# Performance work log

Measured on AMD Instinct MI355X. Metric: run time of the kernel, lower is better.

The kernel has to match this reference:

```python
import jax, jax.numpy as jnp
import numpy as np

ST_HIDDEN = 128
ST_HEADS = 4
ST_LAYERS = 3
RES_SCALE = 1.0
DK = ST_HIDDEN // ST_HEADS


def build_3d_adj(spatial_ei, spatial_ea, n_nodes, window):
    # replicate spatial edges per time slice with node offset t*n_nodes
    offs = (jnp.arange(window) * n_nodes)[None, :, None]  # [1,W,1]
    all_sp_idx = (spatial_ei[:, None, :] + offs).reshape(2, -1)  # [2, W*E]
    all_sp_attr = jnp.tile(spatial_ea, (window, 1))  # [W*E, De]
    # temporal edges t -> t+1 for every node
    src = jnp.arange((window - 1) * n_nodes)
    temp_idx = jnp.stack([src, src + n_nodes], axis=0)  # [2, (W-1)*N]
    temp_attr = jnp.broadcast_to(spatial_ea.mean(axis=0, keepdims=True),
                                 (temp_idx.shape[1], spatial_ea.shape[1]))
    ei = jnp.concatenate([all_sp_idx, temp_idx], axis=1)
    ea = jnp.concatenate([all_sp_attr, temp_attr], axis=0)
    return ei, ea


def seg_softmax(logits, dst, num_nodes):
    # logits [E,H], segment softmax over dst (pyg_softmax)
    m = jax.ops.segment_max(logits, dst, num_segments=num_nodes)  # [N,H]
    ex = jnp.exp(logits - m[dst])
    s = jax.ops.segment_sum(ex, dst, num_segments=num_nodes)
    return ex / (s[dst] + 1e-16)


def layernorm(x, g, b, eps=1e-5):
    mu = x.mean(-1, keepdims=True)
    var = ((x - mu) ** 2).mean(-1, keepdims=True)
    return (x - mu) * jax.lax.rsqrt(var + eps) * g + b


def block(x, ei, ea, qw, qb, kw, kb, vw, vb, fw, fb, ow, ob, ln_g, ln_b):
    B, Nt, _ = x.shape
    H, dk = ST_HEADS, DK
    Q = (x @ qw + qb).reshape(B, Nt, H, dk)
    K = (x @ kw + kb).reshape(B, Nt, H, dk)
    V = (x @ vw + vb).reshape(B, Nt, H, dk)
    src, dst = ei[0], ei[1]
    q_e = Q[:, dst]  # [B,E,H,dk]
    k_e = K[:, src]
    v_e = V[:, src]
    film = ea @ fw + fb  # [E, 2*hidden]
    gamma, beta = jnp.split(film, 2, axis=-1)
    gamma = gamma.reshape(1, -1, H, dk)
    beta = beta.reshape(1, -1, H, dk)
    k_e = k_e * (1.0 + gamma) + beta
    logits = (q_e * k_e).sum(-1) / np.sqrt(dk).astype(np.float32)  # [B,E,H]
    att = jax.vmap(lambda l: seg_softmax(l, dst, Nt))(logits)
    msg = att[..., None] * v_e  # [B,E,H,dk]
    out = jnp.zeros((B, Nt, H, dk), x.dtype).at[:, dst].add(msg)
    y = out.reshape(B, Nt, H * dk) @ ow + ob
    return layernorm(x + y, ln_g, ln_b)


def setup_inputs() -> dict:
    key = jax.random.key(0)
    ks = jax.random.split(key, 12)
    B, W, N, Fin, E, De = 2, 16, 1000, 16, 16000, 8
    H, L = ST_HIDDEN, ST_LAYERS
    g = lambda k, s: jax.random.normal(k, s, jnp.float32) * 0.05
    return {
        "xw": jax.random.normal(ks[0], (B, W, N, Fin), jnp.float32),
        "spatial_ei": jax.random.randint(ks[1], (2, E), 0, N),
        "spatial_ea": jax.random.normal(ks[2], (E, De), jnp.float32),
        "in_w": g(ks[3], (Fin, H)), "in_b": jnp.zeros((H,), jnp.float32),
        "qw": g(ks[4], (L, H, H)), "qb": jnp.zeros((L, H), jnp.float32),
        "kw": g(ks[5], (L, H, H)), "kb": jnp.zeros((L, H), jnp.float32),
        "vw": g(ks[6], (L, H, H)), "vb": jnp.zeros((L, H), jnp.float32),
        "fw": g(ks[7], (L, De, 2 * H)), "fb": jnp.zeros((L, 2 * H), jnp.float32),
        "ow": g(ks[8], (L, H, H)), "ob": jnp.zeros((L, H), jnp.float32),
        "ln_g": jnp.ones((L, H), jnp.float32), "ln_b": jnp.zeros((L, H), jnp.float32),
        "head_w": g(ks[9], (H, 1)), "head_b": jnp.zeros((1,), jnp.float32),
    }


def reference(xw, spatial_ei, spatial_ea, in_w, in_b, qw, qb, kw, kb, vw, vb,
              fw, fb, ow, ob, ln_g, ln_b, head_w, head_b):
    B, W, N, Fin = xw.shape
    ei, ea = build_3d_adj(spatial_ei, spatial_ea, N, W)
    x = xw.reshape(B, W * N, Fin) @ in_w + in_b
    for l in range(ST_LAYERS):
        bx = block(x, ei, ea, qw[l], qb[l], kw[l], kb[l], vw[l], vb[l],
                   fw[l], fb[l], ow[l], ob[l], ln_g[l], ln_b[l])
        x = x + RES_SCALE * (bx - x)
    last = x.reshape(B, W, N, -1)[:, -1]  # [B,N,H]
    return jax.nn.softplus(last @ head_w + head_b).squeeze(-1)  # [B,N]
```

## Files before the change

### kernel.cpp

```cpp
#include <hip/hip_runtime.h>
#include <math.h>

constexpr int B    = 2;
constexpr int W    = 16;
constexpr int N    = 1000;
constexpr int FIN  = 16;
constexpr int E    = 16000;
constexpr int DE   = 8;
constexpr int H    = 128;
constexpr int L    = 3;
constexpr int WL   = 4;
constexpr int W0G  = 12;
constexpr int RPB  = WL * N;
constexpr int ROWS = B * RPB;
constexpr int NMAT = 12;

__device__ __forceinline__ float blockSum128(float v) {
  #pragma unroll
  for (int off = 32; off >= 1; off >>= 1) v += __shfl_xor(v, off);
  __shared__ float s2[2];
  int w = threadIdx.x >> 6;
  __syncthreads();
  if ((threadIdx.x & 63) == 0) s2[w] = v;
  __syncthreads();
  return s2[0] + s2[1];
}

__device__ __forceinline__ float dpp_add_xor1(float x) {
  int y = __builtin_amdgcn_update_dpp(0, __float_as_int(x), 0xB1, 0xF, 0xF, true);
  return x + __int_as_float(y);
}
__device__ __forceinline__ float dpp_add_xor2(float x) {
  int y = __builtin_amdgcn_update_dpp(0, __float_as_int(x), 0x4E, 0xF, 0xF, true);
  return x + __int_as_float(y);
}
__device__ __forceinline__ float headSum32(float p) {
  p = dpp_add_xor1(p);
  p = dpp_add_xor2(p);
  p += __shfl_xor(p, 4);
  p += __shfl_xor(p, 8);
  p += __shfl_xor(p, 16);
  return p;
}
__device__ __forceinline__ float dot4(float4 a, float4 b) {
  return a.x * b.x + a.y * b.y + a.z * b.z + a.w * b.w;
}

__global__ void k_count_scan(const int* __restrict__ ei, int* __restrict__ offs,
                             int* __restrict__ cursor, float* __restrict__ meanea) {
  __shared__ int cnt[N];
  __shared__ int scn[1024];
  int t = threadIdx.x;
  if (t < 8) meanea[t] = 0.f;
  if (t < N) cnt[t] = 0;
  __syncthreads();
  int vals[16];
  int nv = 0;
  for (int e = t; e < E; e += 1024) vals[nv++] = ei[E + e];
  for (int i = 0; i < nv; i++) atomicAdd(&cnt[vals[i]], 1);
  __syncthreads();
  int v = (t < N) ? cnt[t] : 0;
  scn[t] = v;
  __syncthreads();
  for (int st = 1; st < 1024; st <<= 1) {
    int add = (t >= st) ? scn[t - st] : 0;
    __syncthreads();
    scn[t] += add;
    __syncthreads();
  }
  if (t < N) {
    offs[t + 1] = scn[t];
    if (t == 0) offs[0] = 0;
    cursor[t] = scn[t] - v;
  }
}

__global__ void k_prep2(const int* __restrict__ ei, const float* __restrict__ ea,
                        int* __restrict__ cursor, int2* __restrict__ csr,
                        float* __restrict__ meanea,
                        const float* __restrict__ qw, const float* __restrict__ kw,
                        const float* __restrict__ vw, const float* __restrict__ ow,
                        float4* __restrict__ wTp4,
                        const float* __restrict__ xw, const float* __restrict__ in_w,
                        const float* __restrict__ in_b, float* __restrict__ x) {
  int bid = blockIdx.x;
  int t = threadIdx.x;
  if (bid < 64) {
    int e = bid * 256 + t;
    if (e < E) {
      int src = ei[e];
      int dst = ei[E + e];
      int pos = atomicAdd(&cursor[dst], 1);
      csr[pos] = make_int2(src, e);
    }
  } else if (bid < 128) {
    __shared__ float sbuf[256];
    int d = t & 7, g = t >> 3;
    float s = 0.f;
    for (int e = (bid - 64) * 32 + g; e < E; e += 64 * 32) s += ea[e * DE + d];
    sbuf[t] = s;
    __syncthreads();
    for (int st = 16; st >= 1; st >>= 1) {
      if (g < st) sbuf[g * 8 + d] += sbuf[(g + st) * 8 + d];
      __syncthreads();
    }
    if (g == 0) atomicAdd(&meanea[d], sbuf[d]);
  } else if (bid < 128 + NMAT * 16) {
    int bid2 = bid - 128;
    int mat = bid2 / 16;
    int pair = bid2 % 16;
    int kk4 = pair * 2 + (t >> 7);
    int c = t & 127;
    int l = mat >> 2, mm = mat & 3;
    const float* src = ((mm == 0) ? qw : (mm == 1) ? kw : (mm == 2) ? vw : ow) + (long)l * H * H;
    int k0 = kk4 * 4;
    float4 v4;
    v4.x = src[(k0 + 0) * H + c];
    v4.y = src[(k0 + 1) * H + c];
    v4.z = src[(k0 + 2) * H + c];
    v4.w = src[(k0 + 3) * H + c];
    wTp4[((long)mat * 32 + kk4) * H + c] = v4;
  } else {
    int bi = bid - (128 + NMAT * 16);
    int b = bi / 63, tt = bi % 63;
    int lr0 = tt * 64;
    __shared__ float xwS[64][FIN];
    __shared__ float inS[FIN][H];
    for (int i = t; i < 64 * FIN; i += 256) {
      int r = i >> 4, k = i & 15;
      int lr = lr0 + r;
      float val = 0.f;
      if (lr < RPB) {
        int wl = lr / N, n = lr % N;
        val = xw[(((long)b * W + (W0G + wl)) * N + n) * FIN + k];
      }
      xwS[r][k] = val;
    }
    for (int i = t; i < FIN * H; i += 256) inS[i >> 7][i & 127] = in_w[i];
    __syncthreads();
    #pragma unroll
    for (int qi = 0; qi < 8; qi++) {
      int idx = t + qi * 256;
      int r = idx >> 5, cq = idx & 31;
      int lr = lr0 + r;
      if (lr < RPB) {
        float4 acc = *(const float4*)(in_b + cq * 4);
        #pragma unroll
        for (int k = 0; k < FIN; k++) {
          float xv = xwS[r][k];
          float4 w4 = *(const float4*)(&inS[k][cq * 4]);
          acc.x += xv * w4.x; acc.y += xv * w4.y; acc.z += xv * w4.z; acc.w += xv * w4.w;
        }
        *(float4*)(x + ((long)b * RPB + lr) * H + cq * 4) = acc;
      }
    }
  }
}

__global__ void k_film(const float* __restrict__ ea, const float* __restrict__ fw,
                       const float* __restrict__ fb, const float* __restrict__ meanea,
                       unsigned int* __restrict__ filmh) {
  int e0 = blockIdx.x * 4;
  int t = threadIdx.x;
  float rgw[DE], rbw[DE];
  #pragma unroll
  for (int d = 0; d < DE; d++) {
    rgw[d] = fw[d * 2 * H + t];
    rbw[d] = fw[d * 2 * H + H + t];
  }
  float fbg = fb[t], fbb = fb[H + t];
  for (int e = e0; e < e0 + 4 && e <= E; e++) {
    float a[DE];
    if (e < E) {
      float4 a0 = *(const float4*)(ea + (long)e * DE);
      float4 a1 = *(const float4*)(ea + (long)e * DE + 4);
      a[0] = a0.x; a[1] = a0.y; a[2] = a0.z; a[3] = a0.w;
      a[4] = a1.x; a[5] = a1.y; a[6] = a1.z; a[7] = a1.w;
    } else {
      #pragma unroll
      for (int d = 0; d < DE; d++) a[d] = meanea[d] * (1.0f / E);
    }
    float g = fbg, be = fbb;
    #pragma unroll
    for (int d = 0; d < DE; d++) {
      g  += a[d] * rgw[d];
      be += a[d] * rbw[d];
    }
    unsigned int gb = __float_as_uint(g);
    gb = (gb + 0x7fffu + ((gb >> 16) & 1u)) >> 16;
    unsigned int bb_ = __float_as_uint(be);
    bb_ = (bb_ + 0x7fffu + ((bb_ >> 16) & 1u)) & 0xffff0000u;
    filmh[(long)e * H + t] = gb | bb_;
  }
}

__global__ void k_gemm(const float* __restrict__ X, const float4* __restrict__ wTp4,
                       int matBase,
                       const float* __restrict__ bq, const float* __restrict__ bk,
                       const float* __restrict__ bv,
                       float* __restrict__ Cq, float* __restrict__ Ck, float* __restrict__ Cv,
                       int base, int rows_pb, int tiles) {
  int m = blockIdx.y;
  const float* bm = (m == 0) ? bq : (m == 1) ? bk : bv;
  float* Cm       = (m == 0) ? Cq : (m == 1) ? Ck : Cv;
  const float4* wp = wTp4 + (long)(matBase + m) * 32 * H;
  int bb = blockIdx.x / tiles;
  int tt = blockIdx.x % tiles;
  int lr0 = tt * 32;
  long grow0 = (long)bb * RPB + base + lr0;
  int t = threadIdx.x;
  __shared__ float xs[32][H];
  #pragma unroll
  for (int qi = 0; qi < 4; qi++) {
    int idx = t + qi * 256;
    int r = idx >> 5, c4 = idx & 31;
    float4 v4 = make_float4(0.f, 0.f, 0.f, 0.f);
    if (lr0 + r < rows_pb) v4 = *(const float4*)(X + (grow0 + r) * H + c4 * 4);
    *(float4*)&xs[r][c4 * 4] = v4;
  }
  __syncthreads();
  int cg = t & 31, rg = t >> 5;
  float4 bias4 = *(const float4*)(bm + cg * 4);
  float4 acc0 = bias4, acc1 = bias4, acc2 = bias4, acc3 = bias4;
  #pragma unroll 4
  for (int kk4 = 0; kk4 < 32; kk4++) {
    const float4* wr = wp + kk4 * H + cg * 4;
    float4 w0 = wr[0], w1 = wr[1], w2 = wr[2], w3 = wr[3];
    float4 x0 = *(const float4*)&xs[rg * 4 + 0][kk4 * 4];
    float4 x1 = *(const float4*)&xs[rg * 4 + 1][kk4 * 4];
    float4 x2 = *(const float4*)&xs[rg * 4 + 2][kk4 * 4];
    float4 x3 = *(const float4*)&xs[rg * 4 + 3][kk4 * 4];
    acc0.x += dot4(x0, w0); acc0.y += dot4(x0, w1); acc0.z += dot4(x0, w2); acc0.w += dot4(x0, w3);
    acc1.x += dot4(x1, w0); acc1.y += dot4(x1, w1); acc1.z += dot4(x1, w2); acc1.w += dot4(x1, w3);
    acc2.x += dot4(x2, w0); acc2.y += dot4(x2, w1); acc2.z += dot4(x2, w2); acc2.w += dot4(x2, w3);
    acc3.x += dot4(x3, w0); acc3.y += dot4(x3, w1); acc3.z += dot4(x3, w2); acc3.w += dot4(x3, w3);
  }
  int lrr = lr0 + rg * 4;
  if (lrr + 0 < rows_pb) *(float4*)(Cm + (grow0 + rg * 4 + 0) * H + cg * 4) = acc0;
  if (lrr + 1 < rows_pb) *(float4*)(Cm + (grow0 + rg * 4 + 1) * H + cg * 4) = acc1;
  if (lrr + 2 < rows_pb) *(float4*)(Cm + (grow0 + rg * 4 + 2) * H + cg * 4) = acc2;
  if (lrr + 3 < rows_pb) *(float4*)(Cm + (grow0 + rg * 4 + 3) * H + cg * 4) = acc3;
}

__global__ void k_attn_oln(const float* __restrict__ Qb, const float* __restrict__ Kb,
                           const float* __restrict__ Vb,
                           const unsigned int* __restrict__ filmh,
                           const int* __restrict__ offs, const int2* __restrict__ csr,
                           const float* __restrict__ x, const float4* __restrict__ owp,
                           const float* __restrict__ ob, const float* __restrict__ lng,
                           const float* __restrict__ lnb, float* __restrict__ xo,
                           int out_lo,
                           const float* __restrict__ hw, const float* __restrict__ hb,
                           float* __restrict__ out, int do_head) {
  int tid = threadIdx.x;
  int nwin = WL - out_lo;
  int idx = blockIdx.x;
  int b = idx / (nwin * N);
  int rem = idx % (nwin * N);
  int wl = out_lo + rem / N;
  int n = rem % N;
  long drow = ((long)b * WL + wl) * N + n;
  float q = Qb[drow * H + tid];
  long sbase = ((long)b * WL + wl) * N;
  long trow  = ((long)b * WL + wl - 1) * N + n;
  const float scale = 0.17677669529663687f;
  int i0 = offs[n], i1 = offs[n + 1];

  unsigned int fh = filmh[(long)E * H + tid];
  float g  = __uint_as_float(fh << 16);
  float be = __uint_as_float(fh & 0xffff0000u);
  float kv = Kb[trow * H + tid];
  float vv = Vb[trow * H + tid];
  float p  = q * (kv * (1.f + g) + be);
  float pe = __expf(headSum32(p) * scale);
  float ssum = pe, acc = pe * vv;

  for (int i4 = i0; i4 < i1; i4 += 4) {
    #pragma unroll
    for (int j = 0; j < 4; j++) {
      int i = i4 + j;
      int ic = (i < i1) ? i : (i1 - 1);
      int2 se = csr[ic];
      long srow = sbase + se.x;
      unsigned int f2 = filmh[(long)se.y * H + tid];
      float g2 = __uint_as_float(f2 << 16);
      float b2 = __uint_as_float(f2 & 0xffff0000u);
      float kv2 = Kb[srow * H + tid];
      float vv2 = Vb[srow * H + tid];
      float p2  = q * (kv2 * (1.f + g2) + b2);
      float pe2 = __expf(headSum32(p2) * scale);
      pe2 = (i < i1) ? pe2 : 0.f;
      ssum += pe2;
      acc  += pe2 * vv2;
    }
  }
  float ab = acc / (ssum + 1e-16f);

  __shared__ float sab[H];
  sab[tid] = ab;
  __syncthreads();
  float y = ob[tid];
  #pragma unroll 8
  for (int kk4 = 0; kk4 < 32; kk4++) {
    float4 w4 = owp[kk4 * H + tid];
    float4 a4 = *(const float4*)&sab[kk4 * 4];
    y += dot4(a4, w4);
  }

  float v = x[drow * H + tid] + y;
  float mu = blockSum128(v) * (1.f / H);
  float dv = v - mu;
  float var = blockSum128(dv * dv) * (1.f / H);
  float o = dv * rsqrtf(var + 1e-5f) * lng[tid] + lnb[tid];

  if (!do_head) {
    xo[drow * H + tid] = o;
  } else {
    float hv = o * hw[tid];
    float tot = blockSum128(hv);
    if (tid == 0) {
      float z = tot + hb[0];
      out[b * N + n] = fmaxf(z, 0.f) + log1pf(expf(-fabsf(z)));
    }
  }
}

extern "C" void kernel_launch(void* const* d_in, const int* in_sizes, int n_in,
                              void* d_out, int out_size, void* d_ws, size_t ws_size,
                              hipStream_t stream) {
  const float* xw   = (const float*)d_in[0];
  const int*   ei   = (const int*)d_in[1];
  const float* ea   = (const float*)d_in[2];
  const float* in_w = (const float*)d_in[3];
  const float* in_b = (const float*)d_in[4];
  const float* qw   = (const float*)d_in[5];
  const float* qb   = (const float*)d_in[6];
  const float* kw   = (const float*)d_in[7];
  const float* kb   = (const float*)d_in[8];
  const float* vw   = (const float*)d_in[9];
  const float* vb   = (const float*)d_in[10];
  const float* fw   = (const float*)d_in[11];
  const float* fb   = (const float*)d_in[12];
  const float* ow   = (const float*)d_in[13];
  const float* ob   = (const float*)d_in[14];
  const float* ln_g = (const float*)d_in[15];
  const float* ln_b = (const float*)d_in[16];
  const float* hw   = (const float*)d_in[17];
  const float* hb   = (const float*)d_in[18];
  float* out = (float*)d_out;

  float* ws   = (float*)d_ws;
  float* x    = ws;
  float* x2   = x  + (long)ROWS * H;
  float* Qb   = x2 + (long)ROWS * H;
  float* Kb   = Qb + (long)ROWS * H;
  float* Vb   = Kb + (long)ROWS * H;
  float* wTp  = Vb + (long)ROWS * H;
  unsigned int* filmh = (unsigned int*)(wTp + (long)NMAT * H * H);
  float* meanea = (float*)(filmh + (long)(E + 1) * H);
  int* offs    = (int*)(meanea + 8);
  int* cursor  = offs + N + 1;
  int2* csr    = (int2*)(cursor + N);
  float4* wTp4 = (float4*)wTp;

  k_count_scan<<<1, 1024, 0, stream>>>(ei, offs, cursor, meanea);
  k_prep2<<<128 + NMAT * 16 + 126, 256, 0, stream>>>(
      ei, ea, cursor, csr, meanea, qw, kw, vw, ow, wTp4, xw, in_w, in_b, x);

  float* xa = x;
  float* xb = x2;
  for (int l = 0; l < L; l++) {
    int in_lo = l, out_lo = l + 1;
    k_film<<<(E + 1 + 3) / 4, 128, 0, stream>>>(
        ea, fw + (long)l * DE * 2 * H, fb + (long)l * 2 * H, meanea, filmh);
    int rows_pb = (WL - in_lo) * N;
    int tiles = (rows_pb + 31) / 32;
    k_gemm<<<dim3(B * tiles, 3), 256, 0, stream>>>(
        xa, wTp4, l * 4, qb + (long)l * H, kb + (long)l * H, vb + (long)l * H,
        Qb, Kb, Vb, in_lo * N, rows_pb, tiles);
    int nout = B * (WL - out_lo) * N;
    int last = (l == L - 1) ? 1 : 0;
    k_attn_oln<<<nout, H, 0, stream>>>(
        Qb, Kb, Vb, filmh, offs, csr,
        xa, wTp4 + ((long)l * 4 + 3) * 32 * H, ob + (long)l * H,
        ln_g + (long)l * H, ln_b + (long)l * H, xb, out_lo,
        hw, hb, out, last);
    float* tmp = xa; xa = xb; xb = tmp;
  }
}
```

Before: 268.5 us.

## Precompute FiLM for all layers in prep, pack four nodes per attention block

The per-layer FiLM kernel is removed. FiLM coefficients for all three layers are now computed once inside the prep kernel and stored in a three-layer buffer, and the edge-attribute mean moves into a second block of the count/scan kernel so prep can read it without atomics. The attention/out-proj/LayerNorm kernel now processes four destination nodes per 512-thread block, using a grouped block reduction in place of one node per 128-thread block. This cuts kernel launches and small-block scheduling overhead, at the cost of more workspace and a larger prep kernel.

```diff
diff --git a/kernel.cpp b/kernel.cpp
--- a/kernel.cpp
+++ b/kernel.cpp
@@ -14,17 +14,9 @@
 constexpr int RPB  = WL * N;
 constexpr int ROWS = B * RPB;
 constexpr int NMAT = 12;
-
-__device__ __forceinline__ float blockSum128(float v) {
-  #pragma unroll
-  for (int off = 32; off >= 1; off >>= 1) v += __shfl_xor(v, off);
-  __shared__ float s2[2];
-  int w = threadIdx.x >> 6;
-  __syncthreads();
-  if ((threadIdx.x & 63) == 0) s2[w] = v;
-  __syncthreads();
-  return s2[0] + s2[1];
-}
+constexpr int FB   = (E + 1 + 7) / 8;
+constexpr int NPB  = 4;
+constexpr int NG   = N / NPB;
 
 __device__ __forceinline__ float dpp_add_xor1(float x) {
   int y = __builtin_amdgcn_update_dpp(0, __float_as_int(x), 0xB1, 0xF, 0xF, true);
@@ -45,13 +37,36 @@
 __device__ __forceinline__ float dot4(float4 a, float4 b) {
   return a.x * b.x + a.y * b.y + a.z * b.z + a.w * b.w;
 }
+__device__ __forceinline__ float grpSum128(float v, int tid, int g) {
+  #pragma unroll
+  for (int off = 32; off >= 1; off >>= 1) v += __shfl_xor(v, off);
+  __shared__ float sred[8];
+  __syncthreads();
+  if ((tid & 63) == 0) sred[tid >> 6] = v;
+  __syncthreads();
+  return sred[g * 2] + sred[g * 2 + 1];
+}
 
 __global__ void k_count_scan(const int* __restrict__ ei, int* __restrict__ offs,
-                             int* __restrict__ cursor, float* __restrict__ meanea) {
+                             int* __restrict__ cursor,
+                             const float* __restrict__ ea, float* __restrict__ meanea) {
+  int t = threadIdx.x;
+  if (blockIdx.x == 1) {
+    __shared__ float sbuf[1024];
+    int d = t & 7, g = t >> 3;
+    float s = 0.f;
+    for (int e = g; e < E; e += 128) s += ea[(long)e * DE + d];
+    sbuf[t] = s;
+    __syncthreads();
+    for (int st = 64; st >= 1; st >>= 1) {
+      if (g < st) sbuf[g * 8 + d] += sbuf[(g + st) * 8 + d];
+      __syncthreads();
+    }
+    if (g == 0) meanea[d] = sbuf[d];
+    return;
+  }
   __shared__ int cnt[N];
   __shared__ int scn[1024];
-  int t = threadIdx.x;
-  if (t < 8) meanea[t] = 0.f;
   if (t < N) cnt[t] = 0;
   __syncthreads();
   int vals[16];
@@ -77,12 +92,14 @@
 
 __global__ void k_prep2(const int* __restrict__ ei, const float* __restrict__ ea,
                         int* __restrict__ cursor, int2* __restrict__ csr,
-                        float* __restrict__ meanea,
+                        const float* __restrict__ meanea,
                         const float* __restrict__ qw, const float* __restrict__ kw,
                         const float* __restrict__ vw, const float* __restrict__ ow,
                         float4* __restrict__ wTp4,
                         const float* __restrict__ xw, const float* __restrict__ in_w,
-                        const float* __restrict__ in_b, float* __restrict__ x) {
+                        const float* __restrict__ in_b, float* __restrict__ x,
+                        const float* __restrict__ fw, const float* __restrict__ fb,
+                        unsigned int* __restrict__ filmh) {
   int bid = blockIdx.x;
   int t = threadIdx.x;
   if (bid < 64) {
@@ -93,20 +110,8 @@
       int pos = atomicAdd(&cursor[dst], 1);
       csr[pos] = make_int2(src, e);
     }
-  } else if (bid < 128) {
-    __shared__ float sbuf[256];
-    int d = t & 7, g = t >> 3;
-    float s = 0.f;
-    for (int e = (bid - 64) * 32 + g; e < E; e += 64 * 32) s += ea[e * DE + d];
-    sbuf[t] = s;
-    __syncthreads();
-    for (int st = 16; st >= 1; st >>= 1) {
-      if (g < st) sbuf[g * 8 + d] += sbuf[(g + st) * 8 + d];
-      __syncthreads();
-    }
-    if (g == 0) atomicAdd(&meanea[d], sbuf[d]);
-  } else if (bid < 128 + NMAT * 16) {
-    int bid2 = bid - 128;
+  } else if (bid < 64 + NMAT * 16) {
+    int bid2 = bid - 64;
     int mat = bid2 / 16;
     int pair = bid2 % 16;
     int kk4 = pair * 2 + (t >> 7);
@@ -120,8 +125,8 @@
     v4.z = src[(k0 + 2) * H + c];
     v4.w = src[(k0 + 3) * H + c];
     wTp4[((long)mat * 32 + kk4) * H + c] = v4;
-  } else {
-    int bi = bid - (128 + NMAT * 16);
+  } else if (bid < 64 + NMAT * 16 + 126) {
+    int bi = bid - (64 + NMAT * 16);
     int b = bi / 63, tt = bi % 63;
     int lr0 = tt * 64;
     __shared__ float xwS[64][FIN];
@@ -154,43 +159,46 @@
         *(float4*)(x + ((long)b * RPB + lr) * H + cq * 4) = acc;
       }
     }
-  }
-}
-
-__global__ void k_film(const float* __restrict__ ea, const float* __restrict__ fw,
-                       const float* __restrict__ fb, const float* __restrict__ meanea,
-                       unsigned int* __restrict__ filmh) {
-  int e0 = blockIdx.x * 4;
-  int t = threadIdx.x;
-  float rgw[DE], rbw[DE];
-  #pragma unroll
-  for (int d = 0; d < DE; d++) {
-    rgw[d] = fw[d * 2 * H + t];
-    rbw[d] = fw[d * 2 * H + H + t];
-  }
-  float fbg = fb[t], fbb = fb[H + t];
-  for (int e = e0; e < e0 + 4 && e <= E; e++) {
-    float a[DE];
-    if (e < E) {
-      float4 a0 = *(const float4*)(ea + (long)e * DE);
-      float4 a1 = *(const float4*)(ea + (long)e * DE + 4);
-      a[0] = a0.x; a[1] = a0.y; a[2] = a0.z; a[3] = a0.w;
-      a[4] = a1.x; a[5] = a1.y; a[6] = a1.z; a[7] = a1.w;
-    } else {
-      #pragma unroll
-      for (int d = 0; d < DE; d++) a[d] = meanea[d] * (1.0f / E);
-    }
-    float g = fbg, be = fbb;
+  } else {
+    int fi = bid - (64 + NMAT * 16 + 126);
+    int l = fi / FB;
+    int blk = fi % FB;
+    int ch = t & 127;
+    int eg = t >> 7;
+    const float* fwl = fw + (long)l * DE * 2 * H;
+    const float* fbl = fb + (long)l * 2 * H;
+    unsigned int* fh = filmh + (long)l * (E + 1) * H;
+    float rgw[DE], rbw[DE];
     #pragma unroll
     for (int d = 0; d < DE; d++) {
-      g  += a[d] * rgw[d];
-      be += a[d] * rbw[d];
-    }
-    unsigned int gb = __float_as_uint(g);
-    gb = (gb + 0x7fffu + ((gb >> 16) & 1u)) >> 16;
-    unsigned int bb_ = __float_as_uint(be);
-    bb_ = (bb_ + 0x7fffu + ((bb_ >> 16) & 1u)) & 0xffff0000u;
-    filmh[(long)e * H + t] = gb | bb_;
+      rgw[d] = fwl[d * 2 * H + ch];
+      rbw[d] = fwl[d * 2 * H + H + ch];
+    }
+    float fbg = fbl[ch], fbb = fbl[H + ch];
+    int e0 = blk * 8 + eg * 4;
+    for (int e = e0; e < e0 + 4 && e <= E; e++) {
+      float a[DE];
+      if (e < E) {
+        float4 a0 = *(const float4*)(ea + (long)e * DE);
+        float4 a1 = *(const float4*)(ea + (long)e * DE + 4);
+        a[0] = a0.x; a[1] = a0.y; a[2] = a0.z; a[3] = a0.w;
+        a[4] = a1.x; a[5] = a1.y; a[6] = a1.z; a[7] = a1.w;
+      } else {
+        #pragma unroll
+        for (int d = 0; d < DE; d++) a[d] = meanea[d] * (1.0f / E);
+      }
+      float g = fbg, be = fbb;
+      #pragma unroll
+      for (int d = 0; d < DE; d++) {
+        g  += a[d] * rgw[d];
+        be += a[d] * rbw[d];
+      }
+      unsigned int gb = __float_as_uint(g);
+      gb = (gb + 0x7fffu + ((gb >> 16) & 1u)) >> 16;
+      unsigned int bb_ = __float_as_uint(be);
+      bb_ = (bb_ + 0x7fffu + ((bb_ >> 16) & 1u)) & 0xffff0000u;
+      fh[(long)e * H + ch] = gb | bb_;
+    }
   }
 }
 
@@ -253,25 +261,27 @@
                            const float* __restrict__ hw, const float* __restrict__ hb,
                            float* __restrict__ out, int do_head) {
   int tid = threadIdx.x;
+  int g   = tid >> 7;
+  int ch  = tid & 127;
   int nwin = WL - out_lo;
   int idx = blockIdx.x;
-  int b = idx / (nwin * N);
-  int rem = idx % (nwin * N);
-  int wl = out_lo + rem / N;
-  int n = rem % N;
+  int b = idx / (nwin * NG);
+  int rem = idx % (nwin * NG);
+  int wl = out_lo + rem / NG;
+  int n = (rem % NG) * NPB + g;
   long drow = ((long)b * WL + wl) * N + n;
-  float q = Qb[drow * H + tid];
+  float q = Qb[drow * H + ch];
   long sbase = ((long)b * WL + wl) * N;
   long trow  = ((long)b * WL + wl - 1) * N + n;
   const float scale = 0.17677669529663687f;
   int i0 = offs[n], i1 = offs[n + 1];
 
-  unsigned int fh = filmh[(long)E * H + tid];
-  float g  = __uint_as_float(fh << 16);
+  unsigned int fh = filmh[(long)E * H + ch];
+  float gg = __uint_as_float(fh << 16);
   float be = __uint_as_float(fh & 0xffff0000u);
-  float kv = Kb[trow * H + tid];
-  float vv = Vb[trow * H + tid];
-  float p  = q * (kv * (1.f + g) + be);
+  float kv = Kb[trow * H + ch];
+  float vv = Vb[trow * H + ch];
+  float p  = q * (kv * (1.f + gg) + be);
   float pe = __expf(headSum32(p) * scale);
   float ssum = pe, acc = pe * vv;
 
@@ -282,11 +292,11 @@
       int ic = (i < i1) ? i : (i1 - 1);
       int2 se = csr[ic];
       long srow = sbase + se.x;
-      unsigned int f2 = filmh[(long)se.y * H + tid];
+      unsigned int f2 = filmh[(long)se.y * H + ch];
       float g2 = __uint_as_float(f2 << 16);
       float b2 = __uint_as_float(f2 & 0xffff0000u);
-      float kv2 = Kb[srow * H + tid];
-      float vv2 = Vb[srow * H + tid];
+      float kv2 = Kb[srow * H + ch];
+      float vv2 = Vb[srow * H + ch];
       float p2  = q * (kv2 * (1.f + g2) + b2);
       float pe2 = __expf(headSum32(p2) * scale);
       pe2 = (i < i1) ? pe2 : 0.f;
@@ -296,29 +306,29 @@
   }
   float ab = acc / (ssum + 1e-16f);
 
-  __shared__ float sab[H];
-  sab[tid] = ab;
-  __syncthreads();
-  float y = ob[tid];
+  __shared__ float sab[NPB][H];
+  sab[g][ch] = ab;
+  __syncthreads();
+  float y = ob[ch];
   #pragma unroll 8
   for (int kk4 = 0; kk4 < 32; kk4++) {
-    float4 w4 = owp[kk4 * H + tid];
-    float4 a4 = *(const float4*)&sab[kk4 * 4];
+    float4 w4 = owp[kk4 * H + ch];
+    float4 a4 = *(const float4*)&sab[g][kk4 * 4];
     y += dot4(a4, w4);
   }
 
-  float v = x[drow * H + tid] + y;
-  float mu = blockSum128(v) * (1.f / H);
+  float v = x[drow * H + ch] + y;
+  float mu = grpSum128(v, tid, g) * (1.f / H);
   float dv = v - mu;
-  float var = blockSum128(dv * dv) * (1.f / H);
-  float o = dv * rsqrtf(var + 1e-5f) * lng[tid] + lnb[tid];
+  float var = grpSum128(dv * dv, tid, g) * (1.f / H);
+  float o = dv * rsqrtf(var + 1e-5f) * lng[ch] + lnb[ch];
 
   if (!do_head) {
-    xo[drow * H + tid] = o;
+    xo[drow * H + ch] = o;
   } else {
-    float hv = o * hw[tid];
-    float tot = blockSum128(hv);
-    if (tid == 0) {
+    float hv = o * hw[ch];
+    float tot = grpSum128(hv, tid, g);
+    if (ch == 0) {
       float z = tot + hb[0];
       out[b * N + n] = fmaxf(z, 0.f) + log1pf(expf(-fabsf(z)));
     }
@@ -357,31 +367,30 @@
   float* Vb   = Kb + (long)ROWS * H;
   float* wTp  = Vb + (long)ROWS * H;
   unsigned int* filmh = (unsigned int*)(wTp + (long)NMAT * H * H);
-  float* meanea = (float*)(filmh + (long)(E + 1) * H);
+  int2* csr    = (int2*)(filmh + 3L * (E + 1) * H);
+  float* meanea = (float*)(csr + E);
   int* offs    = (int*)(meanea + 8);
   int* cursor  = offs + N + 1;
-  int2* csr    = (int2*)(cursor + N);
   float4* wTp4 = (float4*)wTp;
 
-  k_count_scan<<<1, 1024, 0, stream>>>(ei, offs, cursor, meanea);
-  k_prep2<<<128 + NMAT * 16 + 126, 256, 0, stream>>>(
-      ei, ea, cursor, csr, meanea, qw, kw, vw, ow, wTp4, xw, in_w, in_b, x);
+  k_count_scan<<<2, 1024, 0, stream>>>(ei, offs, cursor, ea, meanea);
+  k_prep2<<<64 + NMAT * 16 + 126 + 3 * FB, 256, 0, stream>>>(
+      ei, ea, cursor, csr, meanea, qw, kw, vw, ow, wTp4, xw, in_w, in_b, x,
+      fw, fb, filmh);
 
   float* xa = x;
   float* xb = x2;
   for (int l = 0; l < L; l++) {
     int in_lo = l, out_lo = l + 1;
-    k_film<<<(E + 1 + 3) / 4, 128, 0, stream>>>(
-        ea, fw + (long)l * DE * 2 * H, fb + (long)l * 2 * H, meanea, filmh);
     int rows_pb = (WL - in_lo) * N;
     int tiles = (rows_pb + 31) / 32;
     k_gemm<<<dim3(B * tiles, 3), 256, 0, stream>>>(
         xa, wTp4, l * 4, qb + (long)l * H, kb + (long)l * H, vb + (long)l * H,
         Qb, Kb, Vb, in_lo * N, rows_pb, tiles);
-    int nout = B * (WL - out_lo) * N;
+    int nout = B * (WL - out_lo) * NG;
     int last = (l == L - 1) ? 1 : 0;
-    k_attn_oln<<<nout, H, 0, stream>>>(
-        Qb, Kb, Vb, filmh, offs, csr,
+    k_attn_oln<<<nout, NPB * H, 0, stream>>>(
+        Qb, Kb, Vb, filmh + (long)l * (E + 1) * H, offs, csr,
         xa, wTp4 + ((long)l * 4 + 3) * 32 * H, ob + (long)l * H,
         ln_g + (long)l * H, ln_b + (long)l * H, xb, out_lo,
         hw, hb, out, last);
```

Measured after the change: 290.6 us. +8.2%, slower.

## Precompute FiLM for all layers in prep kernel and parallelize edge histogram

Applied to the files above, without the earlier changes.

The three per-layer k_film launches are removed; FiLM gamma/beta for all three layers are now computed up front as extra blocks of k_prep2 and stored in a tripled filmh buffer indexed per layer. The single-block count+scan kernel is split into a multi-block global-atomic histogram (which also does the ea mean), preceded by a memset and followed by a single-block scan. This cuts launches inside the layer loop and spreads the histogram across many blocks. The cost is one more memset and scan launch up front and a larger workspace.

```diff
diff --git a/kernel.cpp b/kernel.cpp
--- a/kernel.cpp
+++ b/kernel.cpp
@@ -14,6 +14,7 @@
 constexpr int RPB  = WL * N;
 constexpr int ROWS = B * RPB;
 constexpr int NMAT = 12;
+constexpr int FB   = (E + 1 + 7) / 8;
 
 __device__ __forceinline__ float blockSum128(float v) {
   #pragma unroll
@@ -46,19 +47,32 @@
   return a.x * b.x + a.y * b.y + a.z * b.z + a.w * b.w;
 }
 
-__global__ void k_count_scan(const int* __restrict__ ei, int* __restrict__ offs,
-                             int* __restrict__ cursor, float* __restrict__ meanea) {
-  __shared__ int cnt[N];
+__global__ void k_hist(const int* __restrict__ ei, int* __restrict__ cnt,
+                       const float* __restrict__ ea, float* __restrict__ meanea) {
+  int bid = blockIdx.x;
+  int t = threadIdx.x;
+  if (bid < 64) {
+    int e = bid * 256 + t;
+    if (e < E) atomicAdd(&cnt[ei[E + e]], 1);
+  } else {
+    __shared__ float sbuf[256];
+    int d = t & 7, g = t >> 3;
+    float s = 0.f;
+    for (int e = (bid - 64) * 32 + g; e < E; e += 64 * 32) s += ea[(long)e * DE + d];
+    sbuf[t] = s;
+    __syncthreads();
+    for (int st = 16; st >= 1; st >>= 1) {
+      if (g < st) sbuf[g * 8 + d] += sbuf[(g + st) * 8 + d];
+      __syncthreads();
+    }
+    if (g == 0) atomicAdd(&meanea[d], sbuf[d]);
+  }
+}
+
+__global__ void k_scan(const int* __restrict__ cnt, int* __restrict__ offs,
+                       int* __restrict__ cursor) {
   __shared__ int scn[1024];
   int t = threadIdx.x;
-  if (t < 8) meanea[t] = 0.f;
-  if (t < N) cnt[t] = 0;
-  __syncthreads();
-  int vals[16];
-  int nv = 0;
-  for (int e = t; e < E; e += 1024) vals[nv++] = ei[E + e];
-  for (int i = 0; i < nv; i++) atomicAdd(&cnt[vals[i]], 1);
-  __syncthreads();
   int v = (t < N) ? cnt[t] : 0;
   scn[t] = v;
   __syncthreads();
@@ -77,12 +91,14 @@
 
 __global__ void k_prep2(const int* __restrict__ ei, const float* __restrict__ ea,
                         int* __restrict__ cursor, int2* __restrict__ csr,
-                        float* __restrict__ meanea,
+                        const float* __restrict__ meanea,
                         const float* __restrict__ qw, const float* __restrict__ kw,
                         const float* __restrict__ vw, const float* __restrict__ ow,
                         float4* __restrict__ wTp4,
                         const float* __restrict__ xw, const float* __restrict__ in_w,
-                        const float* __restrict__ in_b, float* __restrict__ x) {
+                        const float* __restrict__ in_b, float* __restrict__ x,
+                        const float* __restrict__ fw, const float* __restrict__ fb,
+                        unsigned int* __restrict__ filmh) {
   int bid = blockIdx.x;
   int t = threadIdx.x;
   if (bid < 64) {
@@ -93,20 +109,8 @@
       int pos = atomicAdd(&cursor[dst], 1);
       csr[pos] = make_int2(src, e);
     }
-  } else if (bid < 128) {
-    __shared__ float sbuf[256];
-    int d = t & 7, g = t >> 3;
-    float s = 0.f;
-    for (int e = (bid - 64) * 32 + g; e < E; e += 64 * 32) s += ea[e * DE + d];
-    sbuf[t] = s;
-    __syncthreads();
-    for (int st = 16; st >= 1; st >>= 1) {
-      if (g < st) sbuf[g * 8 + d] += sbuf[(g + st) * 8 + d];
-      __syncthreads();
-    }
-    if (g == 0) atomicAdd(&meanea[d], sbuf[d]);
-  } else if (bid < 128 + NMAT * 16) {
-    int bid2 = bid - 128;
+  } else if (bid < 64 + NMAT * 16) {
+    int bid2 = bid - 64;
     int mat = bid2 / 16;
     int pair = bid2 % 16;
     int kk4 = pair * 2 + (t >> 7);
@@ -120,8 +124,8 @@
     v4.z = src[(k0 + 2) * H + c];
     v4.w = src[(k0 + 3) * H + c];
     wTp4[((long)mat * 32 + kk4) * H + c] = v4;
-  } else {
-    int bi = bid - (128 + NMAT * 16);
+  } else if (bid < 64 + NMAT * 16 + 126) {
+    int bi = bid - (64 + NMAT * 16);
     int b = bi / 63, tt = bi % 63;
     int lr0 = tt * 64;
     __shared__ float xwS[64][FIN];
@@ -154,43 +158,46 @@
         *(float4*)(x + ((long)b * RPB + lr) * H + cq * 4) = acc;
       }
     }
-  }
-}
-
-__global__ void k_film(const float* __restrict__ ea, const float* __restrict__ fw,
-                       const float* __restrict__ fb, const float* __restrict__ meanea,
-                       unsigned int* __restrict__ filmh) {
-  int e0 = blockIdx.x * 4;
-  int t = threadIdx.x;
-  float rgw[DE], rbw[DE];
-  #pragma unroll
-  for (int d = 0; d < DE; d++) {
-    rgw[d] = fw[d * 2 * H + t];
-    rbw[d] = fw[d * 2 * H + H + t];
-  }
-  float fbg = fb[t], fbb = fb[H + t];
-  for (int e = e0; e < e0 + 4 && e <= E; e++) {
-    float a[DE];
-    if (e < E) {
-      float4 a0 = *(const float4*)(ea + (long)e * DE);
-      float4 a1 = *(const float4*)(ea + (long)e * DE + 4);
-      a[0] = a0.x; a[1] = a0.y; a[2] = a0.z; a[3] = a0.w;
-      a[4] = a1.x; a[5] = a1.y; a[6] = a1.z; a[7] = a1.w;
-    } else {
-      #pragma unroll
-      for (int d = 0; d < DE; d++) a[d] = meanea[d] * (1.0f / E);
-    }
-    float g = fbg, be = fbb;
+  } else {
+    int fi = bid - (64 + NMAT * 16 + 126);
+    int l = fi / FB;
+    int blk = fi % FB;
+    int ch = t & 127;
+    int eg = t >> 7;
+    const float* fwl = fw + (long)l * DE * 2 * H;
+    const float* fbl = fb + (long)l * 2 * H;
+    unsigned int* fh = filmh + (long)l * (E + 1) * H;
+    float rgw[DE], rbw[DE];
     #pragma unroll
     for (int d = 0; d < DE; d++) {
-      g  += a[d] * rgw[d];
-      be += a[d] * rbw[d];
-    }
-    unsigned int gb = __float_as_uint(g);
-    gb = (gb + 0x7fffu + ((gb >> 16) & 1u)) >> 16;
-    unsigned int bb_ = __float_as_uint(be);
-    bb_ = (bb_ + 0x7fffu + ((bb_ >> 16) & 1u)) & 0xffff0000u;
-    filmh[(long)e * H + t] = gb | bb_;
+      rgw[d] = fwl[d * 2 * H + ch];
+      rbw[d] = fwl[d * 2 * H + H + ch];
+    }
+    float fbg = fbl[ch], fbb = fbl[H + ch];
+    int e0 = blk * 8 + eg * 4;
+    for (int e = e0; e < e0 + 4 && e <= E; e++) {
+      float a[DE];
+      if (e < E) {
+        float4 a0 = *(const float4*)(ea + (long)e * DE);
+        float4 a1 = *(const float4*)(ea + (long)e * DE + 4);
+        a[0] = a0.x; a[1] = a0.y; a[2] = a0.z; a[3] = a0.w;
+        a[4] = a1.x; a[5] = a1.y; a[6] = a1.z; a[7] = a1.w;
+      } else {
+        #pragma unroll
+        for (int d = 0; d < DE; d++) a[d] = meanea[d] * (1.0f / E);
+      }
+      float g = fbg, be = fbb;
+      #pragma unroll
+      for (int d = 0; d < DE; d++) {
+        g  += a[d] * rgw[d];
+        be += a[d] * rbw[d];
+      }
+      unsigned int gb = __float_as_uint(g);
+      gb = (gb + 0x7fffu + ((gb >> 16) & 1u)) >> 16;
+      unsigned int bb_ = __float_as_uint(be);
+      bb_ = (bb_ + 0x7fffu + ((bb_ >> 16) & 1u)) & 0xffff0000u;
+      fh[(long)e * H + ch] = gb | bb_;
+    }
   }
 }
 
@@ -357,22 +364,24 @@
   float* Vb   = Kb + (long)ROWS * H;
   float* wTp  = Vb + (long)ROWS * H;
   unsigned int* filmh = (unsigned int*)(wTp + (long)NMAT * H * H);
-  float* meanea = (float*)(filmh + (long)(E + 1) * H);
+  int2* csr    = (int2*)(filmh + 3L * (E + 1) * H);
+  int* cnt     = (int*)(csr + E);
+  float* meanea = (float*)(cnt + N);
   int* offs    = (int*)(meanea + 8);
   int* cursor  = offs + N + 1;
-  int2* csr    = (int2*)(cursor + N);
   float4* wTp4 = (float4*)wTp;
 
-  k_count_scan<<<1, 1024, 0, stream>>>(ei, offs, cursor, meanea);
-  k_prep2<<<128 + NMAT * 16 + 126, 256, 0, stream>>>(
-      ei, ea, cursor, csr, meanea, qw, kw, vw, ow, wTp4, xw, in_w, in_b, x);
+  hipMemsetAsync(cnt, 0, (N + 8) * sizeof(int), stream);
+  k_hist<<<128, 256, 0, stream>>>(ei, cnt, ea, meanea);
+  k_scan<<<1, 1024, 0, stream>>>(cnt, offs, cursor);
+  k_prep2<<<64 + NMAT * 16 + 126 + 3 * FB, 256, 0, stream>>>(
+      ei, ea, cursor, csr, meanea, qw, kw, vw, ow, wTp4, xw, in_w, in_b, x,
+      fw, fb, filmh);
 
   float* xa = x;
   float* xb = x2;
   for (int l = 0; l < L; l++) {
     int in_lo = l, out_lo = l + 1;
-    k_film<<<(E + 1 + 3) / 4, 128, 0, stream>>>(
-        ea, fw + (long)l * DE * 2 * H, fb + (long)l * 2 * H, meanea, filmh);
     int rows_pb = (WL - in_lo) * N;
     int tiles = (rows_pb + 31) / 32;
     k_gemm<<<dim3(B * tiles, 3), 256, 0, stream>>>(
@@ -381,7 +390,7 @@
     int nout = B * (WL - out_lo) * N;
     int last = (l == L - 1) ? 1 : 0;
     k_attn_oln<<<nout, H, 0, stream>>>(
-        Qb, Kb, Vb, filmh, offs, csr,
+        Qb, Kb, Vb, filmh + (long)l * (E + 1) * H, offs, csr,
         xa, wTp4 + ((long)l * 4 + 3) * 32 * H, ob + (long)l * H,
         ln_g + (long)l * H, ln_b + (long)l * H, xb, out_lo,
         hw, hb, out, last);
```

New measurement: 255.1 us. 1.05x faster.
